# Kernel tuning notes

Measured on AMD Instinct MI355X. Metric: run time of the kernel, lower is better.

Reference implementation:

```python
import jax, jax.numpy as jnp
import numpy as np

N_GENES = 50000
EMBED = 256
HIDDEN = 256
N_PAIRS = 500000  # undirected interactions -> 2*N_PAIRS directed edges


def setup_inputs() -> dict:
    key = jax.random.key(0)
    ks = jax.random.split(key, 8)
    pairs = jax.random.randint(ks[0], (N_PAIRS, 2), 0, N_GENES)
    a, b = pairs[:, 0], pairs[:, 1]
    # [[a,b],[b,a]] flattened -> symmetric edge_index [2, 2*N_PAIRS]
    edge_index = jnp.stack([jnp.concatenate([a, b]), jnp.concatenate([b, a])]).astype(jnp.int32)
    gene_ind_vec = jax.random.randint(ks[1], (65536,), 0, N_GENES)
    embedding = jax.random.normal(ks[2], (N_GENES, EMBED), dtype=jnp.float32)
    W1 = jax.random.normal(ks[3], (EMBED, HIDDEN), dtype=jnp.float32) * (1.0 / np.sqrt(EMBED))
    b1 = jnp.zeros((HIDDEN,), dtype=jnp.float32)
    W2 = jax.random.normal(ks[4], (HIDDEN, EMBED), dtype=jnp.float32) * (1.0 / np.sqrt(HIDDEN))
    b2 = jnp.zeros((EMBED,), dtype=jnp.float32)
    return {"gene_ind_vec": gene_ind_vec, "edge_index": edge_index,
            "embedding": embedding, "W1": W1, "b1": b1, "W2": W2, "b2": b2}


def gcn_conv(x, src, dst, W, b, n):
    """PyG GCNConv: h = XW; out = D^{-1/2}(A+I)D^{-1/2} h + b."""
    h = x @ W  # [n, out_dim]
    ones_e = jnp.ones(src.shape[0], dtype=x.dtype)
    # degree with self-loops (+1), aggregated at target nodes
    deg = jax.ops.segment_sum(ones_e, dst, num_segments=n) + 1.0
    dinv = jax.lax.rsqrt(deg)
    norm = dinv[src] * dinv[dst]  # [E]
    agg = jax.ops.segment_sum(h[src] * norm[:, None], dst, num_segments=n)
    # self-loop contribution: dinv[i]^2 * h[i]
    return agg + h * (dinv * dinv)[:, None] + b


def reference(gene_ind_vec, edge_index, embedding, W1, b1, W2, b2):
    src, dst = edge_index[0], edge_index[1]
    n = embedding.shape[0]
    # gene_ind_vec only selects device in the original; all-gene embeddings are the node features
    x = gcn_conv(embedding, src, dst, W1, b1, n)
    x = jax.nn.relu(x)  # dropout is identity in eval mode
    x = gcn_conv(x, src, dst, W2, b2, n)
    return x
```

## Files before the change

### kernel.cpp

```cpp
#include <hip/hip_runtime.h>
#include <stdint.h>


typedef unsigned short u16;
typedef __bf16 bf16x8 __attribute__((ext_vector_type(8)));
typedef float f32x4 __attribute__((ext_vector_type(4)));
typedef unsigned short us8 __attribute__((ext_vector_type(8)));
typedef unsigned short us4 __attribute__((ext_vector_type(4)));

#define BSHIFT 8
#define BSTRIDE 6144
#define EPT 8
#define TILE (256 * EPT)

__device__ __forceinline__ float bf2f(u16 u) {
    union { unsigned i; float f; } c;
    c.i = ((unsigned)u) << 16;
    return c.f;
}
__device__ __forceinline__ u16 f2bf(float f) {
    union { float f; unsigned i; } c;
    c.f = f;
    unsigned i = c.i;
    return (u16)((i + 0x7FFF + ((i >> 16) & 1)) >> 16);
}

__global__ __launch_bounds__(256) void prep_kernel(const float* __restrict__ W1,
        const float* __restrict__ W2, u16* __restrict__ Wt1, u16* __restrict__ Wt2,
        int* __restrict__ bcursor) {
    int t = blockIdx.x * 256 + threadIdx.x;
    int k = t >> 8, nn = t & 255;
    size_t idx = ((size_t)nn << 8) + k;
    Wt1[idx] = f2bf(W1[t]);
    Wt2[idx] = f2bf(W2[t]);
    if (blockIdx.x == 0) bcursor[threadIdx.x] = 0;
}

__global__ __launch_bounds__(256) void scatter_kernel(const int* __restrict__ src,
        const int* __restrict__ dst, int* __restrict__ bcursor,
        int2* __restrict__ rec, int E) {
    __shared__ int cnt[256], lcur[256], gbase[256];
    const int t = threadIdx.x;
    const int base = blockIdx.x * TILE;
    cnt[t] = 0;
    __syncthreads();
    int d[EPT], s[EPT], b[EPT];
#pragma unroll
    for (int k = 0; k < EPT; k++) {
        int e = base + t + k * 256;
        if (e < E) {
            d[k] = dst[e];
            s[k] = src[e];
            b[k] = d[k] >> BSHIFT;
            atomicAdd(&cnt[b[k]], 1);
        } else b[k] = -1;
    }
    __syncthreads();
    int c = cnt[t];
    if (c > 0) gbase[t] = atomicAdd(&bcursor[t], c);
    lcur[t] = 0;
    __syncthreads();
#pragma unroll
    for (int k = 0; k < EPT; k++) {
        if (b[k] >= 0) {
            int r = atomicAdd(&lcur[b[k]], 1);
            rec[(size_t)b[k] * BSTRIDE + gbase[b[k]] + r] = make_int2(d[k], s[k]);
        }
    }
}

__global__ __launch_bounds__(256) void bucket_scan(const int* __restrict__ bcursor,
        int* __restrict__ bbase, int* __restrict__ row_ptr, int NB, int n, int E) {
    __shared__ int sc[256];
    int t = threadIdx.x;
    int v = (t < NB) ? bcursor[t] : 0;
    sc[t] = v;
    __syncthreads();
    for (int off = 1; off < 256; off <<= 1) {
        int u = (t >= off) ? sc[t - off] : 0;
        __syncthreads();
        sc[t] += u;
        __syncthreads();
    }
    if (t < NB) bbase[t] = sc[t] - v;
    if (t == 0) { bbase[NB] = E; row_ptr[n] = E; }
}

__global__ __launch_bounds__(256) void bucket_build(const int2* __restrict__ rec,
        const int* __restrict__ bcursor, const int* __restrict__ bbase,
        int* __restrict__ row_ptr, float* __restrict__ dinv,
        int* __restrict__ csr_src, int n) {
    __shared__ int cnt[256], loff[256], sc[256];
    const int b = blockIdx.x;
    const int t = threadIdx.x;
    const int m = bcursor[b];
    const int base = bbase[b];
    const int2* r = rec + (size_t)b * BSTRIDE;
    cnt[t] = 0;
    __syncthreads();
    for (int i = t; i < m; i += 256)
        atomicAdd(&cnt[r[i].x & 255], 1);
    __syncthreads();
    int c = cnt[t];
    sc[t] = c;
    __syncthreads();
    for (int off = 1; off < 256; off <<= 1) {
        int u = (t >= off) ? sc[t - off] : 0;
        __syncthreads();
        sc[t] += u;
        __syncthreads();
    }
    loff[t] = sc[t] - c;
    int node = (b << BSHIFT) + t;
    if (node < n) {
        row_ptr[node] = base + loff[t];
        dinv[node] = 1.0f / sqrtf((float)c + 1.0f);
    }
    __syncthreads();
    sc[t] = loff[t];
    __syncthreads();
    for (int i = t; i < m; i += 256) {
        int2 e = r[i];
        int idx = atomicAdd(&sc[e.x & 255], 1);
        csr_src[base + idx] = e.y;
    }
}

template<bool AF32>
__global__ __launch_bounds__(256, 4) void mfma_gemm(const void* __restrict__ Ap,
        const u16* __restrict__ Wt, const float* __restrict__ dinv,
        u16* __restrict__ g, int M) {
    __shared__ u16 As[128][40];
    __shared__ u16 Bs[128][40];
    const int tid = threadIdx.x;
    const int row0 = blockIdx.x * 128;
    const int col0 = blockIdx.y * 128;

    const int lane = tid & 63;
    const int w = tid >> 6;
    const int wr = w >> 1, wc = w & 1;
    const int l15 = lane & 15, kg = lane >> 4;

    f32x4 acc[4][4];
#pragma unroll
    for (int mi = 0; mi < 4; mi++)
#pragma unroll
        for (int ni = 0; ni < 4; ni++)
            acc[mi][ni] = (f32x4){0.f, 0.f, 0.f, 0.f};

    const int srow = tid >> 1;
    const int shalf = tid & 1;
    const int grow = row0 + srow;

    for (int k0 = 0; k0 < 256; k0 += 32) {
        if (AF32) {
            const float* srcp = (const float*)Ap + ((size_t)grow << 8) + k0 + shalf * 16;
            float4 v[4];
#pragma unroll
            for (int q = 0; q < 4; q++)
                v[q] = (grow < M) ? *(const float4*)(srcp + q * 4)
                                  : make_float4(0.f, 0.f, 0.f, 0.f);
            u16 tmp[16];
#pragma unroll
            for (int q = 0; q < 4; q++) {
                tmp[q * 4 + 0] = f2bf(v[q].x); tmp[q * 4 + 1] = f2bf(v[q].y);
                tmp[q * 4 + 2] = f2bf(v[q].z); tmp[q * 4 + 3] = f2bf(v[q].w);
            }
            *(us8*)&As[srow][shalf * 16]     = *(us8*)&tmp[0];
            *(us8*)&As[srow][shalf * 16 + 8] = *(us8*)&tmp[8];
        } else {
            const u16* srcp = (const u16*)Ap + ((size_t)grow << 8) + k0 + shalf * 16;
            us8 z = {0, 0, 0, 0, 0, 0, 0, 0};
            us8 a0 = (grow < M) ? *(const us8*)srcp       : z;
            us8 a1 = (grow < M) ? *(const us8*)(srcp + 8) : z;
            *(us8*)&As[srow][shalf * 16]     = a0;
            *(us8*)&As[srow][shalf * 16 + 8] = a1;
        }
        {
            const u16* srcp = Wt + (((size_t)(col0 + srow)) << 8) + k0 + shalf * 16;
            *(us8*)&Bs[srow][shalf * 16]     = *(const us8*)srcp;
            *(us8*)&Bs[srow][shalf * 16 + 8] = *(const us8*)(srcp + 8);
        }
        __syncthreads();
        bf16x8 af[4], bfv[4];
#pragma unroll
        for (int mi = 0; mi < 4; mi++)
            af[mi] = *(const bf16x8*)&As[wr * 64 + mi * 16 + l15][kg * 8];
#pragma unroll
        for (int ni = 0; ni < 4; ni++)
            bfv[ni] = *(const bf16x8*)&Bs[wc * 64 + ni * 16 + l15][kg * 8];
#pragma unroll
        for (int mi = 0; mi < 4; mi++)
#pragma unroll
            for (int ni = 0; ni < 4; ni++)
                acc[mi][ni] = __builtin_amdgcn_mfma_f32_16x16x32_bf16(
                    af[mi], bfv[ni], acc[mi][ni], 0, 0, 0);
        __syncthreads();
    }

#pragma unroll
    for (int mi = 0; mi < 4; mi++) {
#pragma unroll
        for (int r = 0; r < 4; r++) {
            int gr = row0 + wr * 64 + mi * 16 + kg * 4 + r;
            if (gr < M) {
                float s = dinv[gr];
                u16* dstp = g + ((size_t)gr << 8) + col0 + wc * 64 + l15;
#pragma unroll
                for (int ni = 0; ni < 4; ni++)
                    dstp[ni * 16] = f2bf(acc[mi][ni][r] * s);
            }
        }
    }
}

template<bool OUT16>
__global__ __launch_bounds__(256) void agg_kernel(const u16* __restrict__ g,
        const int* __restrict__ csr_src, const int* __restrict__ row_ptr,
        const float* __restrict__ dinv, const float* __restrict__ bias,
        void* __restrict__ outp, int n, int do_relu) {
    int wid = threadIdx.x >> 6;
    int lane = threadIdx.x & 63;
    int node = blockIdx.x * 4 + wid;
    if (node >= n) return;
    int jb = row_ptr[node], je = row_ptr[node + 1];
    const size_t co = (size_t)(lane * 4);
    float4 a0 = make_float4(0.f, 0.f, 0.f, 0.f);
    float4 a1 = make_float4(0.f, 0.f, 0.f, 0.f);
    int j = jb;
    for (; j + 8 <= je; j += 8) {
        int s0 = csr_src[j + 0], s1 = csr_src[j + 1];
        int s2 = csr_src[j + 2], s3 = csr_src[j + 3];
        int s4 = csr_src[j + 4], s5 = csr_src[j + 5];
        int s6 = csr_src[j + 6], s7 = csr_src[j + 7];
        ushort4 v0 = *(const ushort4*)(g + ((size_t)s0 << 8) + co);
        ushort4 v1 = *(const ushort4*)(g + ((size_t)s1 << 8) + co);
        ushort4 v2 = *(const ushort4*)(g + ((size_t)s2 << 8) + co);
        ushort4 v3 = *(const ushort4*)(g + ((size_t)s3 << 8) + co);
        ushort4 v4 = *(const ushort4*)(g + ((size_t)s4 << 8) + co);
        ushort4 v5 = *(const ushort4*)(g + ((size_t)s5 << 8) + co);
        ushort4 v6 = *(const ushort4*)(g + ((size_t)s6 << 8) + co);
        ushort4 v7 = *(const ushort4*)(g + ((size_t)s7 << 8) + co);
        a0.x += bf2f(v0.x); a0.y += bf2f(v0.y); a0.z += bf2f(v0.z); a0.w += bf2f(v0.w);
        a1.x += bf2f(v1.x); a1.y += bf2f(v1.y); a1.z += bf2f(v1.z); a1.w += bf2f(v1.w);
        a0.x += bf2f(v2.x); a0.y += bf2f(v2.y); a0.z += bf2f(v2.z); a0.w += bf2f(v2.w);
        a1.x += bf2f(v3.x); a1.y += bf2f(v3.y); a1.z += bf2f(v3.z); a1.w += bf2f(v3.w);
        a0.x += bf2f(v4.x); a0.y += bf2f(v4.y); a0.z += bf2f(v4.z); a0.w += bf2f(v4.w);
        a1.x += bf2f(v5.x); a1.y += bf2f(v5.y); a1.z += bf2f(v5.z); a1.w += bf2f(v5.w);
        a0.x += bf2f(v6.x); a0.y += bf2f(v6.y); a0.z += bf2f(v6.z); a0.w += bf2f(v6.w);
        a1.x += bf2f(v7.x); a1.y += bf2f(v7.y); a1.z += bf2f(v7.z); a1.w += bf2f(v7.w);
    }
    for (; j < je; ++j) {
        int s = csr_src[j];
        ushort4 v = *(const ushort4*)(g + ((size_t)s << 8) + co);
        a0.x += bf2f(v.x); a0.y += bf2f(v.y); a0.z += bf2f(v.z); a0.w += bf2f(v.w);
    }
    ushort4 gd = *(const ushort4*)(g + ((size_t)node << 8) + co);
    float dn = dinv[node];
    float4 bv = *(const float4*)(bias + co);
    float4 o;
    o.x = (a0.x + a1.x + bf2f(gd.x)) * dn + bv.x;
    o.y = (a0.y + a1.y + bf2f(gd.y)) * dn + bv.y;
    o.z = (a0.z + a1.z + bf2f(gd.z)) * dn + bv.z;
    o.w = (a0.w + a1.w + bf2f(gd.w)) * dn + bv.w;
    if (do_relu) {
        o.x = fmaxf(o.x, 0.f); o.y = fmaxf(o.y, 0.f);
        o.z = fmaxf(o.z, 0.f); o.w = fmaxf(o.w, 0.f);
    }
    if (OUT16) {
        us4 ov = { f2bf(o.x), f2bf(o.y), f2bf(o.z), f2bf(o.w) };
        *(us4*)((u16*)outp + ((size_t)node << 8) + co) = ov;
    } else {
        *(float4*)((float*)outp + ((size_t)node << 8) + co) = o;
    }
}

extern "C" void kernel_launch(void* const* d_in, const int* in_sizes, int n_in,
                              void* d_out, int out_size, void* d_ws, size_t ws_size,
                              hipStream_t stream) {
    const int*   edge_index = (const int*)d_in[1];
    const float* embedding  = (const float*)d_in[2];
    const float* W1 = (const float*)d_in[3];
    const float* b1 = (const float*)d_in[4];
    const float* W2 = (const float*)d_in[5];
    const float* b2 = (const float*)d_in[6];

    const int E = in_sizes[1] / 2;
    const int n = in_sizes[2] / 256;
    const int* src = edge_index;
    const int* dst = edge_index + E;
    const int NB = (n + 255) >> BSHIFT;

    char* ws = (char*)d_ws;
    int* row_ptr = (int*)ws;    ws += ((size_t)n + 1) * 4;
    float* dinv = (float*)ws;   ws += (size_t)n * 4;
    int* bcursor = (int*)ws;    ws += 256 * 4;
    int* bbase = (int*)ws;      ws += 257 * 4;
    int* csr_src = (int*)ws;    ws += (size_t)E * 4;
    u16* Wt1 = (u16*)ws;        ws += 65536 * 2;
    u16* Wt2 = (u16*)ws;        ws += 65536 * 2;
    ws = (char*)(((uintptr_t)ws + 127) & ~(uintptr_t)127);
    int2* rec = (int2*)ws;      ws += (size_t)NB * BSTRIDE * 8;
    ws = (char*)(((uintptr_t)ws + 127) & ~(uintptr_t)127);
    u16* g = (u16*)ws;
    u16* x1 = (u16*)d_out;

    prep_kernel<<<256, 256, 0, stream>>>(W1, W2, Wt1, Wt2, bcursor);
    scatter_kernel<<<(E + TILE - 1) / TILE, 256, 0, stream>>>(src, dst, bcursor, rec, E);
    bucket_scan<<<1, 256, 0, stream>>>(bcursor, bbase, row_ptr, NB, n, E);
    bucket_build<<<NB, 256, 0, stream>>>(rec, bcursor, bbase, row_ptr, dinv, csr_src, n);

    dim3 gg((n + 127) / 128, 2);
    mfma_gemm<true><<<gg, 256, 0, stream>>>(embedding, Wt1, dinv, g, n);
    agg_kernel<true><<<(n + 3) / 4, 256, 0, stream>>>(g, csr_src, row_ptr, dinv, b1, x1, n, 1);
    mfma_gemm<false><<<gg, 256, 0, stream>>>(x1, Wt2, dinv, g, n);
    agg_kernel<false><<<(n + 3) / 4, 256, 0, stream>>>(g, csr_src, row_ptr, dinv, b2, (float*)d_out, n, 0);
}
```

Baseline: 241.9 us.

## Fuse weight prep into scatter, fold bucket scan into build, pack edge records

Measured after the change: 245.7 us. No clear change (+1.5%).

```diff
diff --git a/kernel.cpp b/kernel.cpp
--- a/kernel.cpp
+++ b/kernel.cpp
@@ -25,22 +25,20 @@
     return (u16)((i + 0x7FFF + ((i >> 16) & 1)) >> 16);
 }
 
-__global__ __launch_bounds__(256) void prep_kernel(const float* __restrict__ W1,
-        const float* __restrict__ W2, u16* __restrict__ Wt1, u16* __restrict__ Wt2,
-        int* __restrict__ bcursor) {
-    int t = blockIdx.x * 256 + threadIdx.x;
-    int k = t >> 8, nn = t & 255;
-    size_t idx = ((size_t)nn << 8) + k;
-    Wt1[idx] = f2bf(W1[t]);
-    Wt2[idx] = f2bf(W2[t]);
-    if (blockIdx.x == 0) bcursor[threadIdx.x] = 0;
-}
-
 __global__ __launch_bounds__(256) void scatter_kernel(const int* __restrict__ src,
         const int* __restrict__ dst, int* __restrict__ bcursor,
-        int2* __restrict__ rec, int E) {
+        unsigned* __restrict__ rec, int E,
+        const float* __restrict__ W1, const float* __restrict__ W2,
+        u16* __restrict__ Wt1, u16* __restrict__ Wt2) {
     __shared__ int cnt[256], lcur[256], gbase[256];
     const int t = threadIdx.x;
+    if (blockIdx.x < 256) {
+        int wt = blockIdx.x * 256 + t;
+        int k = wt >> 8, nn = wt & 255;
+        size_t idx = ((size_t)nn << 8) + k;
+        Wt1[idx] = f2bf(W1[wt]);
+        Wt2[idx] = f2bf(W2[wt]);
+    }
     const int base = blockIdx.x * TILE;
     cnt[t] = 0;
     __syncthreads();
@@ -64,42 +62,39 @@
     for (int k = 0; k < EPT; k++) {
         if (b[k] >= 0) {
             int r = atomicAdd(&lcur[b[k]], 1);
-            rec[(size_t)b[k] * BSTRIDE + gbase[b[k]] + r] = make_int2(d[k], s[k]);
+            rec[(size_t)b[k] * BSTRIDE + gbase[b[k]] + r] =
+                ((unsigned)(d[k] & 255) << 16) | (unsigned)s[k];
         }
     }
 }
 
-__global__ __launch_bounds__(256) void bucket_scan(const int* __restrict__ bcursor,
-        int* __restrict__ bbase, int* __restrict__ row_ptr, int NB, int n, int E) {
-    __shared__ int sc[256];
-    int t = threadIdx.x;
-    int v = (t < NB) ? bcursor[t] : 0;
-    sc[t] = v;
-    __syncthreads();
-    for (int off = 1; off < 256; off <<= 1) {
-        int u = (t >= off) ? sc[t - off] : 0;
-        __syncthreads();
-        sc[t] += u;
-        __syncthreads();
-    }
-    if (t < NB) bbase[t] = sc[t] - v;
-    if (t == 0) { bbase[NB] = E; row_ptr[n] = E; }
-}
-
-__global__ __launch_bounds__(256) void bucket_build(const int2* __restrict__ rec,
-        const int* __restrict__ bcursor, const int* __restrict__ bbase,
-        int* __restrict__ row_ptr, float* __restrict__ dinv,
-        int* __restrict__ csr_src, int n) {
+__global__ __launch_bounds__(256) void bucket_build(const unsigned* __restrict__ rec,
+        const int* __restrict__ bcursor, int* __restrict__ row_ptr,
+        float* __restrict__ dinv, int* __restrict__ csr_src,
+        int n, int NB, int E) {
     __shared__ int cnt[256], loff[256], sc[256];
     const int b = blockIdx.x;
     const int t = threadIdx.x;
-    const int m = bcursor[b];
-    const int base = bbase[b];
-    const int2* r = rec + (size_t)b * BSTRIDE;
+    int bv = (t < NB) ? bcursor[t] : 0;
+    sc[t] = bv;
+    __syncthreads();
+    for (int off = 1; off < 256; off <<= 1) {
+        int u = (t >= off) ? sc[t - off] : 0;
+        __syncthreads();
+        sc[t] += u;
+        __syncthreads();
+    }
+    __shared__ int base_s, m_s;
+    if (t == b) { base_s = sc[t] - bv; m_s = bv; }
+    if (b == 0 && t == 0) row_ptr[n] = E;
+    __syncthreads();
+    const int m = m_s;
+    const int base = base_s;
+    const unsigned* r = rec + (size_t)b * BSTRIDE;
     cnt[t] = 0;
     __syncthreads();
     for (int i = t; i < m; i += 256)
-        atomicAdd(&cnt[r[i].x & 255], 1);
+        atomicAdd(&cnt[r[i] >> 16], 1);
     __syncthreads();
     int c = cnt[t];
     sc[t] = c;
@@ -120,9 +115,9 @@
     sc[t] = loff[t];
     __syncthreads();
     for (int i = t; i < m; i += 256) {
-        int2 e = r[i];
-        int idx = atomicAdd(&sc[e.x & 255], 1);
-        csr_src[base + idx] = e.y;
+        unsigned e = r[i];
+        int idx = atomicAdd(&sc[e >> 16], 1);
+        csr_src[base + idx] = (int)(e & 0xFFFFu);
     }
 }
 
@@ -295,20 +290,19 @@
     int* row_ptr = (int*)ws;    ws += ((size_t)n + 1) * 4;
     float* dinv = (float*)ws;   ws += (size_t)n * 4;
     int* bcursor = (int*)ws;    ws += 256 * 4;
-    int* bbase = (int*)ws;      ws += 257 * 4;
     int* csr_src = (int*)ws;    ws += (size_t)E * 4;
     u16* Wt1 = (u16*)ws;        ws += 65536 * 2;
     u16* Wt2 = (u16*)ws;        ws += 65536 * 2;
     ws = (char*)(((uintptr_t)ws + 127) & ~(uintptr_t)127);
-    int2* rec = (int2*)ws;      ws += (size_t)NB * BSTRIDE * 8;
+    unsigned* rec = (unsigned*)ws; ws += (size_t)NB * BSTRIDE * 4;
     ws = (char*)(((uintptr_t)ws + 127) & ~(uintptr_t)127);
     u16* g = (u16*)ws;
     u16* x1 = (u16*)d_out;
 
-    prep_kernel<<<256, 256, 0, stream>>>(W1, W2, Wt1, Wt2, bcursor);
-    scatter_kernel<<<(E + TILE - 1) / TILE, 256, 0, stream>>>(src, dst, bcursor, rec, E);
-    bucket_scan<<<1, 256, 0, stream>>>(bcursor, bbase, row_ptr, NB, n, E);
-    bucket_build<<<NB, 256, 0, stream>>>(rec, bcursor, bbase, row_ptr, dinv, csr_src, n);
+    hipMemsetAsync(bcursor, 0, 256 * 4, stream);
+    scatter_kernel<<<(E + TILE - 1) / TILE, 256, 0, stream>>>(src, dst, bcursor, rec, E,
+                                                              W1, W2, Wt1, Wt2);
+    bucket_build<<<NB, 256, 0, stream>>>(rec, bcursor, row_ptr, dinv, csr_src, n, NB, E);
 
     dim3 gg((n + 127) / 128, 2);
     mfma_gemm<true><<<gg, 256, 0, stream>>>(embedding, Wt1, dinv, g, n);
```
